# Performance work log

Measured on AMD Instinct MI355X. Metric: run time of the kernel, lower is better.

## Reference

```python
import jax, jax.numpy as jnp
import numpy as np

BLOCK_H = 1
BLOCK_W = 1
EPS = 1e-6


def setup_inputs() -> dict:
    key = jax.random.key(0)
    ks = jax.random.split(key, 8)
    B, L, D = 2, 4096, 1024
    NBF, DK = 16, 64  # nb_features, d_k (d_model // n_heads)
    ws = 1.0 / np.sqrt(D)  # nn.Linear-like init scale
    return {
        "q": jax.random.normal(ks[0], (B, L, D), jnp.float32),
        "k": jax.random.normal(ks[1], (B, L, D), jnp.float32),
        "v": jax.random.normal(ks[2], (B, L, D), jnp.float32),
        "w_q": jax.random.normal(ks[3], (D, D), jnp.float32) * ws,
        "w_k": jax.random.normal(ks[4], (D, D), jnp.float32) * ws,
        "w_v": jax.random.normal(ks[5], (D, D), jnp.float32) * ws,
        "w_o": jax.random.normal(ks[6], (D, D), jnp.float32) * ws,
        "omega": jax.random.normal(ks[7], (NBF, DK), jnp.float32) / np.sqrt(DK),
    }


def reference(q, k, v, w_q, w_k, w_v, w_o, omega):
    B, Lq, D = q.shape
    Lk = k.shape[1]
    NBF, DK = omega.shape
    H = D // DK

    # projections (torch nn.Linear: x @ W.T), split into heads
    qh = (q @ w_q.T).reshape(B, Lq, H, DK)
    kh = (k @ w_k.T).reshape(B, Lk, H, DK)
    vh = (v @ w_v.T).reshape(B, Lk, H, DK)

    qp = jnp.exp(-0.5 * jnp.square(jnp.einsum('blhd,fd->blhf', qh, omega)))
    kp = jnp.exp(-0.5 * jnp.square(jnp.einsum('blhd,fd->blhf', kh, omega)))
    qp = qp / (qp.sum(-1, keepdims=True) + EPS)
    kp = kp / (kp.sum(-1, keepdims=True) + EPS)

    # causal prefix sums over key positions
    K_cum = jnp.cumsum(kp, axis=1)                                    # [B,Lk,H,F]
    KV_cum = jnp.cumsum(kp[..., None] * vh[..., None, :], axis=1)     # [B,Lk,H,F,DK]

    # blockwise causal key index per query position
    q_idx = jnp.arange(Lq)
    key_idx = jnp.clip((q_idx // BLOCK_H + 1) * BLOCK_W - 1, 0, Lk - 1)
    K_sel = K_cum[:, key_idx]      # [B,Lq,H,F]
    KV_sel = KV_cum[:, key_idx]    # [B,Lq,H,F,DK]

    numerator = jnp.einsum('blhf,blhfd->blhd', qp, KV_sel)
    denominator = jnp.sum(qp * K_sel, axis=-1, keepdims=True)
    out = (numerator / (denominator + EPS)).reshape(B, Lq, D)
    return out @ w_o.T
```

## Files before the change

kernel.cpp:

```cpp
#include <hip/hip_runtime.h>

#define L_SEQ   4096
#define BATCH   2
#define DMODEL  1024
#define HEADS   16
#define DKH     64
#define NBF     16
#define CHUNK   64
#define NCHUNK  64
#define NCHAIN  32
#define STATE_SZ 1040
#define EPSF    1e-6f

typedef __attribute__((ext_vector_type(8))) __bf16 bf16x8;
typedef __attribute__((ext_vector_type(4))) float  floatx4;

__device__ __forceinline__ unsigned short f2bf(float x) {
  unsigned u = __builtin_bit_cast(unsigned, x);
  u += 0x7fffu + ((u >> 16) & 1u);
  return (unsigned short)(u >> 16);
}
__device__ __forceinline__ float bf2f(unsigned short u) {
  return __builtin_bit_cast(float, ((unsigned)u) << 16);
}

#define GLOAD16(gp, lp) \
  __builtin_amdgcn_global_load_lds((const __attribute__((address_space(1))) void*)(gp), \
                                   (__attribute__((address_space(3))) void*)(lp), 16, 0, 0)

__global__ __launch_bounds__(256) void prep(const float* __restrict__ wv, const float* __restrict__ wo,
                                            const float* __restrict__ wq, const float* __restrict__ wk,
                                            const float* __restrict__ omega,
                                            unsigned short* __restrict__ wvb, unsigned short* __restrict__ wob,
                                            unsigned short* __restrict__ wtq, unsigned short* __restrict__ wtk) {
  __shared__ float ws[64 * 64];
  __shared__ float oms[NBF * 64];
  const int blk = blockIdx.x;
  const int tid = threadIdx.x;
  if (blk < 2048) {
    const float* in = (blk < 1024) ? wv : wo;
    unsigned short* out = (blk < 1024) ? wvb : wob;
    int i = (blk & 1023) * 256 + tid;
    float4 v4 = ((const float4*)in)[i];
    ushort4 o;
    o.x = f2bf(v4.x); o.y = f2bf(v4.y); o.z = f2bf(v4.z); o.w = f2bf(v4.w);
    ((ushort4*)out)[i] = o;
    return;
  }
  const int local = blk - 2048;
  const int z = local >> 8;
  const int h = (local & 255) >> 4;
  const int s = local & 15;
  const float* w = z ? wk : wq;
  unsigned short* wt = z ? wtk : wtq;
  for (int i = tid; i < 64 * 64; i += 256) {
    int r = i >> 6, c = i & 63;
    ws[i] = w[(size_t)(h * 64 + r) * DMODEL + s * 64 + c];
  }
  for (int i = tid; i < NBF * 64; i += 256) oms[i] = omega[i];
  __syncthreads();
  for (int j = tid; j < NBF * 64; j += 256) {
    int f = j >> 6, c = j & 63;
    float acc = 0.f;
#pragma unroll
    for (int d = 0; d < 64; ++d) acc += oms[f * 64 + d] * ws[d * 64 + c];
    wt[(size_t)(h * NBF + f) * DMODEL + s * 64 + c] = f2bf(acc);
  }
}

__global__ __launch_bounds__(256) void proj_all(const float* __restrict__ q, const float* __restrict__ k,
                                                const float* __restrict__ v,
                                                const unsigned short* __restrict__ wtq,
                                                const unsigned short* __restrict__ wtk,
                                                const unsigned short* __restrict__ wvb,
                                                float* __restrict__ qp_t, float* __restrict__ kp_t,
                                                unsigned short* __restrict__ vh) {
  constexpr int K = DMODEL;
  __shared__ char smem[24576];
  float* As = (float*)smem;
  unsigned short* Bs = (unsigned short*)(smem + 16384);

  const int tid  = threadIdx.x;
  const int wave = tid >> 6, lane = tid & 63;

  const int bid = blockIdx.x;
  const int id = (bid & 7) * 96 + (bid >> 3);
  int op, mt, nt;
  const float* A;
  const unsigned short* Bt;
  if (id < 256) {
    op = id >> 7;
    const int local = id & 127;
    nt = (local & 1) << 7;
    mt = (local >> 1) << 7;
    A  = op ? k : q;
    Bt = op ? wtk : wtq;
  } else {
    op = 2;
    const int local = id - 256;
    nt = (local & 7) << 7;
    mt = (local >> 3) << 7;
    A  = v;
    Bt = wvb;
  }

  const int wm = (wave >> 1) << 6, wn = (wave & 1) << 6;
  const int r16 = lane & 15, kg = lane >> 4;

  floatx4 acc[4][4];
#pragma unroll
  for (int m = 0; m < 4; ++m)
#pragma unroll
    for (int n = 0; n < 4; ++n) acc[m][n] = floatx4{0.f, 0.f, 0.f, 0.f};

  const int arow = wave * 32 + (lane >> 3);
  const int acolsw = ((lane & 7) ^ (lane >> 3)) << 2;
  const float* aG = A + (size_t)(mt + arow) * K + acolsw;
  const int brow = wave * 16 + (lane >> 2);
  const int bcolsw = (((lane & 3) ^ ((lane >> 3) & 3)) << 3);
  const unsigned short* bG = Bt + (size_t)(nt + brow) * K + bcolsw;

  for (int kt = 0; kt < K; kt += 32) {
#pragma unroll
    for (int j = 0; j < 4; ++j)
      GLOAD16(aG + (size_t)(8 * j) * K + kt, smem + wave * 4096 + j * 1024);
    GLOAD16(bG + kt, (char*)Bs + wave * 1024);
    GLOAD16(bG + (size_t)64 * K + kt, (char*)Bs + 4096 + wave * 1024);
    __syncthreads();

    bf16x8 af[4], bfr[4];
#pragma unroll
    for (int m = 0; m < 4; ++m) {
      const int row = wm + m * 16 + r16;
      const int sA = (kg << 1) ^ (r16 & 7);
      floatx4 lo = *(const floatx4*)(smem + row * 128 + sA * 16);
      floatx4 hi = *(const floatx4*)(smem + row * 128 + (sA ^ 1) * 16);
#pragma unroll
      for (int t2 = 0; t2 < 4; ++t2) {
        af[m][t2]     = (__bf16)lo[t2];
        af[m][4 + t2] = (__bf16)hi[t2];
      }
    }
#pragma unroll
    for (int n = 0; n < 4; ++n) {
      const int row = wn + n * 16 + r16;
      const int sB = kg ^ ((r16 >> 1) & 3);
      bfr[n] = *(const bf16x8*)((char*)Bs + row * 64 + sB * 16);
    }
#pragma unroll
    for (int m = 0; m < 4; ++m)
#pragma unroll
      for (int n = 0; n < 4; ++n)
        acc[m][n] = __builtin_amdgcn_mfma_f32_16x16x32_bf16(af[m], bfr[n], acc[m][n], 0, 0, 0);
    __syncthreads();
  }

  if (op < 2) {
    float* xp_t = op ? kp_t : qp_t;
    const int hbase = (nt + wn) >> 4;
#pragma unroll
    for (int m = 0; m < 4; ++m) {
#pragma unroll
      for (int n = 0; n < 4; ++n) {
        const int hglob = hbase + n;
#pragma unroll
        for (int r = 0; r < 4; ++r) {
          float x = acc[m][n][r];
          float p = __expf(-0.5f * x * x);
          float s = p;
          s += __shfl_xor(s, 1);
          s += __shfl_xor(s, 2);
          s += __shfl_xor(s, 4);
          s += __shfl_xor(s, 8);
          float o = p / (s + EPSF);
          const int row = mt + wm + m * 16 + kg * 4 + r;
          const int b = row >> 12, l = row & 4095;
          xp_t[(((size_t)(b * HEADS + hglob)) * L_SEQ + l) * NBF + r16] = o;
        }
      }
    }
  } else {
#pragma unroll
    for (int m = 0; m < 4; ++m) {
      const int row0 = mt + wm + m * 16 + kg * 4;
#pragma unroll
      for (int n = 0; n < 4; ++n) {
        const int col = nt + wn + n * 16 + r16;
#pragma unroll
        for (int r = 0; r < 4; ++r)
          vh[(size_t)(row0 + r) * DMODEL + col] = f2bf(acc[m][n][r]);
      }
    }
  }
}

__global__ __launch_bounds__(256) void gemm_o(const unsigned short* __restrict__ A,
                                              const unsigned short* __restrict__ Bt,
                                              float* __restrict__ C) {
  constexpr int K = DMODEL;
  __shared__ unsigned short As[128 * 32];
  __shared__ unsigned short Bs[128 * 32];
  const int tid  = threadIdx.x;
  const int wave = tid >> 6, lane = tid & 63;
  const int bid = blockIdx.x;
  const int id = (bid & 7) * 64 + (bid >> 3);
  const int nt = (id & 7) << 7, mt = (id >> 3) << 7;
  const int wm = (wave >> 1) << 6, wn = (wave & 1) << 6;
  const int r16 = lane & 15, kg = lane >> 4;

  floatx4 acc[4][4];
#pragma unroll
  for (int m = 0; m < 4; ++m)
#pragma unroll
    for (int n = 0; n < 4; ++n) acc[m][n] = floatx4{0.f, 0.f, 0.f, 0.f};

  const int ldrow = wave * 16 + (lane >> 2);
  const int ldcolsw = (((lane & 3) ^ ((lane >> 3) & 3)) << 3);
  const unsigned short* aG = A  + (size_t)(mt + ldrow) * K + ldcolsw;
  const unsigned short* bG = Bt + (size_t)(nt + ldrow) * K + ldcolsw;

  for (int kt = 0; kt < K; kt += 32) {
    GLOAD16(aG + kt, (char*)As + wave * 1024);
    GLOAD16(aG + (size_t)64 * K + kt, (char*)As + 4096 + wave * 1024);
    GLOAD16(bG + kt, (char*)Bs + wave * 1024);
    GLOAD16(bG + (size_t)64 * K + kt, (char*)Bs + 4096 + wave * 1024);
    __syncthreads();

    bf16x8 af[4], bfr[4];
#pragma unroll
    for (int m = 0; m < 4; ++m) {
      const int row = wm + m * 16 + r16;
      const int sA = kg ^ ((r16 >> 1) & 3);
      af[m] = *(const bf16x8*)((char*)As + row * 64 + sA * 16);
    }
#pragma unroll
    for (int n = 0; n < 4; ++n) {
      const int row = wn + n * 16 + r16;
      const int sB = kg ^ ((r16 >> 1) & 3);
      bfr[n] = *(const bf16x8*)((char*)Bs + row * 64 + sB * 16);
    }
#pragma unroll
    for (int m = 0; m < 4; ++m)
#pragma unroll
      for (int n = 0; n < 4; ++n)
        acc[m][n] = __builtin_amdgcn_mfma_f32_16x16x32_bf16(af[m], bfr[n], acc[m][n], 0, 0, 0);
    __syncthreads();
  }

#pragma unroll
  for (int m = 0; m < 4; ++m) {
    const int row0 = mt + wm + m * 16 + kg * 4;
#pragma unroll
    for (int n = 0; n < 4; ++n) {
      const int col = nt + wn + n * 16 + r16;
#pragma unroll
      for (int r = 0; r < 4; ++r)
        C[(size_t)(row0 + r) * DMODEL + col] = acc[m][n][r];
    }
  }
}

__global__ __launch_bounds__(64) void scan_chunk_sum(const float* __restrict__ kp_t,
                                                     const unsigned short* __restrict__ vh,
                                                     float* __restrict__ Sws) {
  const int c = blockIdx.x & (NCHUNK - 1);
  const int chain = blockIdx.x >> 6;
  const int b = chain >> 4, h = chain & 15;
  const int d = threadIdx.x;
  __shared__ float kp_s[CHUNK * NBF];
  const float* kpB = kp_t + ((size_t)chain * L_SEQ + c * CHUNK) * NBF;
  for (int i = 0; i < 16; ++i) kp_s[d + i * 64] = kpB[d + i * 64];
  __syncthreads();
  float S[NBF];
#pragma unroll
  for (int f = 0; f < NBF; ++f) S[f] = 0.f;
  const unsigned short* vB = vh + ((size_t)(b * L_SEQ + c * CHUNK)) * DMODEL + h * DKH + d;
  for (int l = 0; l < CHUNK; ++l) {
    float vv = bf2f(vB[(size_t)l * DMODEL]);
#pragma unroll
    for (int f = 0; f < NBF; ++f) S[f] += kp_s[l * NBF + f] * vv;
  }
  float* out = Sws + ((size_t)chain * NCHUNK + c) * STATE_SZ;
#pragma unroll
  for (int f = 0; f < NBF; ++f) out[f * 64 + d] = S[f];
  if (d < NBF) {
    float ks = 0.f;
    for (int l = 0; l < CHUNK; ++l) ks += kp_s[l * NBF + d];
    out[1024 + d] = ks;
  }
}

__global__ __launch_bounds__(64) void scan_chunks(float* __restrict__ Sws) {
  const int chain = blockIdx.x;
  const int e = blockIdx.y * 64 + threadIdx.x;
  if (e >= STATE_SZ) return;
  float acc = 0.f;
  float* p = Sws + (size_t)chain * NCHUNK * STATE_SZ + e;
  for (int c = 0; c < NCHUNK; ++c) {
    float v = p[(size_t)c * STATE_SZ];
    p[(size_t)c * STATE_SZ] = acc;
    acc += v;
  }
}

__global__ __launch_bounds__(64) void scan_apply(const float* __restrict__ qp_t,
                                                 const float* __restrict__ kp_t,
                                                 const unsigned short* __restrict__ vh,
                                                 const float* __restrict__ Sws,
                                                 unsigned short* __restrict__ attn) {
  const int c = blockIdx.x & (NCHUNK - 1);
  const int chain = blockIdx.x >> 6;
  const int b = chain >> 4, h = chain & 15;
  const int d = threadIdx.x;
  __shared__ float kp_s[CHUNK * NBF];
  __shared__ float qp_s[CHUNK * NBF];
  {
    const float* kpB = kp_t + ((size_t)chain * L_SEQ + c * CHUNK) * NBF;
    const float* qpB = qp_t + ((size_t)chain * L_SEQ + c * CHUNK) * NBF;
    for (int i = 0; i < 16; ++i) {
      kp_s[d + i * 64] = kpB[d + i * 64];
      qp_s[d + i * 64] = qpB[d + i * 64];
    }
  }
  __syncthreads();
  const float* st = Sws + ((size_t)chain * NCHUNK + c) * STATE_SZ;
  float S[NBF], kc[NBF];
#pragma unroll
  for (int f = 0; f < NBF; ++f) S[f] = st[f * 64 + d];
#pragma unroll
  for (int f = 0; f < NBF; ++f) kc[f] = st[1024 + f];
  const unsigned short* vB = vh + ((size_t)(b * L_SEQ + c * CHUNK)) * DMODEL + h * DKH + d;
  unsigned short* oB = attn + ((size_t)(b * L_SEQ + c * CHUNK)) * DMODEL + h * DKH + d;
  for (int l = 0; l < CHUNK; ++l) {
    float vv = bf2f(vB[(size_t)l * DMODEL]);
    float num = 0.f, den = 0.f;
#pragma unroll
    for (int f = 0; f < NBF; ++f) {
      float kpf = kp_s[l * NBF + f];
      S[f]  += kpf * vv;
      kc[f] += kpf;
      float qpf = qp_s[l * NBF + f];
      num += qpf * S[f];
      den += qpf * kc[f];
    }
    oB[(size_t)l * DMODEL] = f2bf(num / (den + EPSF));
  }
}

extern "C" void kernel_launch(void* const* d_in, const int* in_sizes, int n_in,
                              void* d_out, int out_size, void* d_ws, size_t ws_size,
                              hipStream_t stream) {
  const float* q   = (const float*)d_in[0];
  const float* k   = (const float*)d_in[1];
  const float* v   = (const float*)d_in[2];
  const float* w_q = (const float*)d_in[3];
  const float* w_k = (const float*)d_in[4];
  const float* w_v = (const float*)d_in[5];
  const float* w_o = (const float*)d_in[6];
  const float* omega = (const float*)d_in[7];
  float* out = (float*)d_out;

  constexpr size_t NQ = (size_t)BATCH * L_SEQ * DMODEL;
  constexpr size_t NW = (size_t)DMODEL * DMODEL;
  constexpr size_t NWT = (size_t)HEADS * NBF * DMODEL;
  constexpr size_t NP = (size_t)BATCH * HEADS * L_SEQ * NBF;
  constexpr size_t NS = (size_t)NCHAIN * NCHUNK * STATE_SZ;

  char* ws = (char*)d_ws;
  size_t off = 0;
  auto alc = [&](size_t bytes) { void* p = ws + off; off += (bytes + 255) & ~(size_t)255; return p; };
  unsigned short* wvb = (unsigned short*)alc(NW * 2);
  unsigned short* wob = (unsigned short*)alc(NW * 2);
  unsigned short* wtq = (unsigned short*)alc(NWT * 2);
  unsigned short* wtk = (unsigned short*)alc(NWT * 2);
  unsigned short* vh  = (unsigned short*)alc(NQ * 2);
  unsigned short* attn = (unsigned short*)alc(NQ * 2);
  float* qp  = (float*)alc(NP * 4);
  float* kp  = (float*)alc(NP * 4);
  float* Sws = (float*)alc(NS * 4);

  prep<<<2560, 256, 0, stream>>>(w_v, w_o, w_q, w_k, omega, wvb, wob, wtq, wtk);
  proj_all<<<768, 256, 0, stream>>>(q, k, v, wtq, wtk, wvb, qp, kp, vh);

  scan_chunk_sum<<<NCHAIN * NCHUNK, 64, 0, stream>>>(kp, vh, Sws);
  scan_chunks<<<dim3(NCHAIN, (STATE_SZ + 63) / 64), 64, 0, stream>>>(Sws);
  scan_apply<<<NCHAIN * NCHUNK, 64, 0, stream>>>(qp, kp, vh, Sws, attn);

  gemm_o<<<512, 256, 0, stream>>>(attn, wob, out);
}
```

Before: 167.5 us.

## Double-buffer LDS tiles in projection and output GEMMs; interleave QK and V tiles

```diff
diff --git a/kernel.cpp b/kernel.cpp
--- a/kernel.cpp
+++ b/kernel.cpp
@@ -75,31 +75,30 @@
                                                 const unsigned short* __restrict__ wvb,
                                                 float* __restrict__ qp_t, float* __restrict__ kp_t,
                                                 unsigned short* __restrict__ vh) {
-  constexpr int K = DMODEL;
-  __shared__ char smem[24576];
-  float* As = (float*)smem;
-  unsigned short* Bs = (unsigned short*)(smem + 16384);
+  constexpr int K = DMODEL, NT = K / 32;
+  __shared__ char smem[2][24576];
 
   const int tid  = threadIdx.x;
   const int wave = tid >> 6, lane = tid & 63;
 
   const int bid = blockIdx.x;
   const int id = (bid & 7) * 96 + (bid >> 3);
+  const int g = id / 3, r3 = id - g * 3;
   int op, mt, nt;
   const float* A;
   const unsigned short* Bt;
-  if (id < 256) {
-    op = id >> 7;
-    const int local = id & 127;
+  if (r3 == 2) {
+    op = g & 1;
+    const int local = g >> 1;
     nt = (local & 1) << 7;
     mt = (local >> 1) << 7;
     A  = op ? k : q;
     Bt = op ? wtk : wtq;
   } else {
     op = 2;
-    const int local = id - 256;
-    nt = (local & 7) << 7;
-    mt = (local >> 3) << 7;
+    const int vt = g * 2 + r3;
+    nt = (vt & 7) << 7;
+    mt = (vt >> 3) << 7;
     A  = v;
     Bt = wvb;
   }
@@ -120,21 +119,23 @@
   const int bcolsw = (((lane & 3) ^ ((lane >> 3) & 3)) << 3);
   const unsigned short* bG = Bt + (size_t)(nt + brow) * K + bcolsw;
 
-  for (int kt = 0; kt < K; kt += 32) {
+  auto stage = [&](int buf, int kt) {
+    char* base = smem[buf];
 #pragma unroll
     for (int j = 0; j < 4; ++j)
-      GLOAD16(aG + (size_t)(8 * j) * K + kt, smem + wave * 4096 + j * 1024);
-    GLOAD16(bG + kt, (char*)Bs + wave * 1024);
-    GLOAD16(bG + (size_t)64 * K + kt, (char*)Bs + 4096 + wave * 1024);
-    __syncthreads();
-
+      GLOAD16(aG + (size_t)(8 * j) * K + kt, base + wave * 4096 + j * 1024);
+    GLOAD16(bG + kt, base + 16384 + wave * 1024);
+    GLOAD16(bG + (size_t)64 * K + kt, base + 16384 + 4096 + wave * 1024);
+  };
+  auto compute = [&](int buf) {
+    const char* base = smem[buf];
     bf16x8 af[4], bfr[4];
 #pragma unroll
     for (int m = 0; m < 4; ++m) {
       const int row = wm + m * 16 + r16;
       const int sA = (kg << 1) ^ (r16 & 7);
-      floatx4 lo = *(const floatx4*)(smem + row * 128 + sA * 16);
-      floatx4 hi = *(const floatx4*)(smem + row * 128 + (sA ^ 1) * 16);
+      floatx4 lo = *(const floatx4*)(base + row * 128 + sA * 16);
+      floatx4 hi = *(const floatx4*)(base + row * 128 + (sA ^ 1) * 16);
 #pragma unroll
       for (int t2 = 0; t2 < 4; ++t2) {
         af[m][t2]     = (__bf16)lo[t2];
@@ -145,13 +146,20 @@
     for (int n = 0; n < 4; ++n) {
       const int row = wn + n * 16 + r16;
       const int sB = kg ^ ((r16 >> 1) & 3);
-      bfr[n] = *(const bf16x8*)((char*)Bs + row * 64 + sB * 16);
+      bfr[n] = *(const bf16x8*)(base + 16384 + row * 64 + sB * 16);
     }
 #pragma unroll
     for (int m = 0; m < 4; ++m)
 #pragma unroll
       for (int n = 0; n < 4; ++n)
         acc[m][n] = __builtin_amdgcn_mfma_f32_16x16x32_bf16(af[m], bfr[n], acc[m][n], 0, 0, 0);
+  };
+
+  stage(0, 0);
+  __syncthreads();
+  for (int t = 0; t < NT; ++t) {
+    if (t + 1 < NT) stage((t + 1) & 1, (t + 1) * 32);
+    compute(t & 1);
     __syncthreads();
   }
 
@@ -197,9 +205,8 @@
 __global__ __launch_bounds__(256) void gemm_o(const unsigned short* __restrict__ A,
                                               const unsigned short* __restrict__ Bt,
                                               float* __restrict__ C) {
-  constexpr int K = DMODEL;
-  __shared__ unsigned short As[128 * 32];
-  __shared__ unsigned short Bs[128 * 32];
+  constexpr int K = DMODEL, NT = K / 32;
+  __shared__ char smem[2][16384];
   const int tid  = threadIdx.x;
   const int wave = tid >> 6, lane = tid & 63;
   const int bid = blockIdx.x;
@@ -219,31 +226,40 @@
   const unsigned short* aG = A  + (size_t)(mt + ldrow) * K + ldcolsw;
   const unsigned short* bG = Bt + (size_t)(nt + ldrow) * K + ldcolsw;
 
-  for (int kt = 0; kt < K; kt += 32) {
-    GLOAD16(aG + kt, (char*)As + wave * 1024);
-    GLOAD16(aG + (size_t)64 * K + kt, (char*)As + 4096 + wave * 1024);
-    GLOAD16(bG + kt, (char*)Bs + wave * 1024);
-    GLOAD16(bG + (size_t)64 * K + kt, (char*)Bs + 4096 + wave * 1024);
-    __syncthreads();
-
+  auto stage = [&](int buf, int kt) {
+    char* base = smem[buf];
+    GLOAD16(aG + kt, base + wave * 1024);
+    GLOAD16(aG + (size_t)64 * K + kt, base + 4096 + wave * 1024);
+    GLOAD16(bG + kt, base + 8192 + wave * 1024);
+    GLOAD16(bG + (size_t)64 * K + kt, base + 8192 + 4096 + wave * 1024);
+  };
+  auto compute = [&](int buf) {
+    const char* base = smem[buf];
     bf16x8 af[4], bfr[4];
 #pragma unroll
     for (int m = 0; m < 4; ++m) {
       const int row = wm + m * 16 + r16;
       const int sA = kg ^ ((r16 >> 1) & 3);
-      af[m] = *(const bf16x8*)((char*)As + row * 64 + sA * 16);
+      af[m] = *(const bf16x8*)(base + row * 64 + sA * 16);
     }
 #pragma unroll
     for (int n = 0; n < 4; ++n) {
       const int row = wn + n * 16 + r16;
       const int sB = kg ^ ((r16 >> 1) & 3);
-      bfr[n] = *(const bf16x8*)((char*)Bs + row * 64 + sB * 16);
+      bfr[n] = *(const bf16x8*)(base + 8192 + row * 64 + sB * 16);
     }
 #pragma unroll
     for (int m = 0; m < 4; ++m)
 #pragma unroll
       for (int n = 0; n < 4; ++n)
         acc[m][n] = __builtin_amdgcn_mfma_f32_16x16x32_bf16(af[m], bfr[n], acc[m][n], 0, 0, 0);
+  };
+
+  stage(0, 0);
+  __syncthreads();
+  for (int t = 0; t < NT; ++t) {
+    if (t + 1 < NT) stage((t + 1) & 1, (t + 1) * 32);
+    compute(t & 1);
     __syncthreads();
   }
 
```

Result: faster. 145.1 us (-13.4%).
